# Optimization experiments

Measured on AMD Instinct MI355X. Metric: run time of the kernel, lower is better.

The kernel has to match this reference:

```python
import jax, jax.numpy as jnp
import numpy as np

G = 16       # groups
GRID = 25    # hardcoded self.grid
EPS = 1e-5   # BatchNorm eps


def _gconv(x, w, pad):
    # x: (B, Cin, H, W), w: (Cout, Cin//G, kh, kw); grouped conv, stride 1
    return jax.lax.conv_general_dilated(
        x, w, window_strides=(1, 1), padding=[(pad, pad), (pad, pad)],
        feature_group_count=G)


def _bn_relu(h, g, b, m, v):
    # h: (G, B, C, H, W); per-group-instance BN params: (G, C). Inference BN.
    scale = (g / jnp.sqrt(v + EPS))[:, None, :, None, None]
    return jax.nn.relu((h - m[:, None, :, None, None]) * scale + b[:, None, :, None, None])


def setup_inputs() -> dict:
    key = jax.random.key(0)
    ks = jax.random.split(key, 11)
    B, C, H, W = 2, 256, 24, 24
    AC = GRID * C  # 6400 affinity channels
    return {
        "x":  jax.random.normal(ks[0], (B, C, H, W), jnp.float32),
        "W1": jax.random.normal(ks[1], (G, C, C // G, 3, 3), jnp.float32) * 0.05,
        "g1": jax.random.uniform(ks[2], (G, C), jnp.float32, 0.5, 1.5),
        "b1": jax.random.normal(ks[3], (G, C), jnp.float32) * 0.1,
        "m1": jax.random.normal(ks[4], (G, C), jnp.float32) * 0.1,
        "v1": jax.random.uniform(ks[5], (G, C), jnp.float32, 0.5, 1.5),
        "W2": jax.random.normal(ks[6], (G, AC, C // G, 1, 1), jnp.float32) * 0.05,
        "g2": jax.random.uniform(ks[7], (G, AC), jnp.float32, 0.5, 1.5),
        "b2": jax.random.normal(ks[8], (G, AC), jnp.float32) * 0.1,
        "m2": jax.random.normal(ks[9], (G, AC), jnp.float32) * 0.1,
        "v2": jax.random.uniform(ks[10], (G, AC), jnp.float32, 0.5, 1.5),
    }


def reference(x, W1, g1, b1, m1, v1, W2, g2, b2, m2, v2):
    B, C, H, W = x.shape
    Cg = C // G
    # 16 independent grouped 3x3 convs over the same input, batched via vmap
    h1 = jax.vmap(lambda w: _gconv(x, w, 1))(W1)          # (G, B, C, H, W)
    h1 = _bn_relu(h1, g1, b1, m1, v1)
    # grouped 1x1 conv with padding=1 (faithful to source -> spatial grows to H+2, W+2)
    a = jax.vmap(lambda h, w: _gconv(h, w, 1))(h1, W2)    # (G, B, 25C, H+2, W+2)
    a = _bn_relu(a, g2, b2, m2, v2)
    pooled = a.mean(axis=(-2, -1))                        # adaptive avg pool -> (G, B, 25C)
    xv = pooled.reshape(G, B, G, GRID * Cg)               # (G, B, G, 25*Cg)
    aff = jnp.einsum('ibkm,iblm->ibkl', xv, xv)           # (G, B, G, G) = theta @ phi
    idx = jnp.arange(G)
    aff_i = aff[idx, :, idx, :] / G                       # aff[:, i], /N  -> (G, B, G)
    ex = h1.reshape(G, B, G, Cg * H * W)
    # torch.matmul((B,G), (B,G,M)) broadcasts 2-D lhs -> (B, B, M); kept faithfully
    z = jnp.einsum('ipk,iqkm->ipqm', aff_i, ex)           # (G, B, B, Cg*H*W)
    z = z.reshape(G, B, B, Cg, H, W).transpose(1, 0, 2, 3, 4, 5)
    return z.reshape(B, G * B * Cg, H, W)                 # (B, B*C, H, W)
```

## Files before the change

kernel.cpp:

```cpp
#include <hip/hip_runtime.h>
#include <hip/hip_bf16.h>


typedef __attribute__((ext_vector_type(8))) short short8;
typedef __attribute__((ext_vector_type(4))) float f32x4;

static __device__ __forceinline__ unsigned short f2bf(float x) {
    unsigned u = __float_as_uint(x);
    unsigned r = (u + 0x7fffu + ((u >> 16) & 1u)) >> 16;
    return (unsigned short)r;
}

#define WA_OFF   33696
#define HS_OFF   40096
#define WLB_OFF  63136
#define B2_OFF   75936
#define PACC_OFF 77536
#define S1_OFF   79136
#define BB1_OFF  79200
#define ZP_OFF   79264
#define SMEM_BYTES 79280

__global__ __launch_bounds__(256) void k12_fused(
    const float* __restrict__ xin,
    const float* __restrict__ W1,
    const float* __restrict__ g1, const float* __restrict__ b1,
    const float* __restrict__ m1, const float* __restrict__ v1,
    const float* __restrict__ W2,
    const float* __restrict__ g2, const float* __restrict__ b2,
    const float* __restrict__ m2, const float* __restrict__ v2,
    unsigned short* __restrict__ h1b,
    float* __restrict__ pooled)
{
    __shared__ __align__(16) char smem[SMEM_BYTES];
    short* xs    = (short*)smem;
    short* wAp   = (short*)(smem + WA_OFF);
    short* hsb   = (short*)(smem + HS_OFF);
    short* wlb   = (short*)(smem + WLB_OFF);
    float* bias2 = (float*)(smem + B2_OFF);
    float* pacc  = (float*)(smem + PACC_OFF);
    float* scale1 = (float*)(smem + S1_OFF);
    float* bias1  = (float*)(smem + BB1_OFF);

    int bid = blockIdx.x;
    int i = bid >> 5, b = (bid >> 4) & 1, g = bid & 15;
    int t = threadIdx.x;

    if (t < 16) {
        int c = i*256 + g*16 + t;
        float sc = g1[c] * rsqrtf(v1[c] + 1e-5f);
        scale1[t] = sc;
        bias1[t]  = b1[c] - m1[c] * sc;
    }
    {
        int* xz = (int*)xs;
        for (int idx = t; idx < 1512; idx += 256) {
            int c = idx / 12, j = idx - (idx / 12) * 12;
            int row, col;
            if (c < 26)      { row = 0;  col = c; }
            else if (c < 52) { row = 25; col = c - 26; }
            else if (c < 78) { row = 26; col = c - 52; }
            else { int k = c - 78; row = 1 + (k >> 1); col = (k & 1) ? 25 : 0; }
            xz[(row*26 + col)*12 + j] = 0;
        }
        if (t < 4) ((int*)(smem + ZP_OFF))[t] = 0;
    }
    {
        const float* xb = &xin[(b*256 + g*16)*576];
        for (int idx = t; idx < 9216; idx += 256) {
            int ci = idx / 576; int s = idx - ci*576;
            int y = s / 24; int x = s - y*24;
            xs[((y+1)*26 + (x+1))*24 + ci] = (short)f2bf(xb[idx]);
        }
    }
    {
        const float* wb = &W1[(i*256 + g*16)*144];
        for (int idx = t; idx < 2560; idx += 256) {
            int kk = idx >> 9, rem = idx & 511, co = rem >> 5, k = rem & 31;
            int tap = 2*kk + (k >> 4), ci = k & 15;
            int c = i*256 + g*16 + co;
            float sc = g1[c] * rsqrtf(v1[c] + 1e-5f);
            float val = (tap < 9) ? wb[co*144 + ci*9 + tap] * sc : 0.f;
            wAp[(kk*16 + co)*40 + k] = (short)f2bf(val);
        }
    }
    for (int m = t; m < 400; m += 256) {
        pacc[m] = 0.f;
        int o = i*6400 + g*400 + m;
        float s2 = g2[o] * rsqrtf(v2[o] + 1e-5f);
        bias2[m] = b2[o] - m2[o] * s2;
        const float4* wr = (const float4*)&W2[o*16];
#pragma unroll
        for (int q = 0; q < 4; q++) {
            float4 wv = wr[q];
            wlb[m*16 + q*4 + 0] = (short)f2bf(wv.x * s2);
            wlb[m*16 + q*4 + 1] = (short)f2bf(wv.y * s2);
            wlb[m*16 + q*4 + 2] = (short)f2bf(wv.z * s2);
            wlb[m*16 + q*4 + 3] = (short)f2bf(wv.w * s2);
        }
    }
    __syncthreads();

    int l = t & 63, w = t >> 6;
    int quad = l >> 4, rc = l & 15;

    f32x4 dreg[9];
    {
        int ci0 = (quad & 1) * 8;
        short8 afr[5];
#pragma unroll
        for (int kk = 0; kk < 5; kk++)
            afr[kk] = *(const short8*)&wAp[(kk*16 + rc)*40 + quad*8];
        f32x4 cb1 = *(const f32x4*)&bias1[quad*4];

        const int offE[5] = {0, 48, 648, 1248, 1296};
        const int offO[5] = {24, 624, 672, 1272, 1872};
        int off[5];
#pragma unroll
        for (int kk = 0; kk < 5; kk++) off[kk] = (quad >= 2) ? offO[kk] : offE[kk];

#pragma unroll
        for (int tt = 0; tt < 9; tt++) {
            int s = (w*9 + tt)*16 + rc;
            int y = s / 24; int x = s - y*24;
            int base = (y*26 + x)*24 + ci0;
            f32x4 acc = cb1;
#pragma unroll
            for (int kk = 0; kk < 5; kk++) {
                short8 bf = *(const short8*)&xs[base + off[kk]];
                acc = __builtin_amdgcn_mfma_f32_16x16x32_bf16(afr[kk], bf, acc, 0, 0, 0);
            }
#pragma unroll
            for (int r = 0; r < 4; r++) acc[r] = fmaxf(acc[r], 0.f);
            dreg[tt] = acc;
        }
    }

    {
        unsigned short* hout = &h1b[((i*2 + b)*256 + g*16)*576];
#pragma unroll
        for (int tt = 0; tt < 9; tt++) {
            int s = (w*9 + tt)*16 + rc;
            f32x4 acc = dreg[tt];
            unsigned short e0 = f2bf(acc[0]), e1 = f2bf(acc[1]);
            unsigned short e2 = f2bf(acc[2]), e3 = f2bf(acc[3]);
            uint2 pk = {(unsigned)e0 | ((unsigned)e1 << 16),
                        (unsigned)e2 | ((unsigned)e3 << 16)};
            *(uint2*)&hsb[s*20 + quad*4] = pk;
            hout[(quad*4 + 0)*576 + s] = e0;
            hout[(quad*4 + 1)*576 + s] = e1;
            hout[(quad*4 + 2)*576 + s] = e2;
            hout[(quad*4 + 3)*576 + s] = e3;
        }
    }

    {
        int q8 = (quad & 1) * 8;
        short8 af2[9];
#pragma unroll
        for (int u = 0; u < 9; u++) {
            int boff = (l < 32) ? (HS_OFF + (((w*9 + u)*16 + rc)*20 + q8)*2) : ZP_OFF;
            af2[u] = *(const short8*)(smem + boff);
        }
        for (int mt = 0; mt < 25; mt++) {
            int m0 = mt*16;
            int woff = (l < 32) ? (WLB_OFF + ((m0 + rc)*16 + q8)*2) : ZP_OFF;
            short8 wf = *(const short8*)(smem + woff);
            float be = bias2[m0 + rc];
            f32x4 cb = {be, be, be, be};

            f32x4 accv = {0.f, 0.f, 0.f, 0.f};
#pragma unroll
            for (int u = 0; u < 9; u++) {
                f32x4 d = __builtin_amdgcn_mfma_f32_16x16x32_bf16(af2[u], wf, cb, 0, 0, 0);
#pragma unroll
                for (int r = 0; r < 4; r++)
                    accv[r] += fmaxf(d[r], 0.f);
            }
            float a = (accv[0] + accv[1]) + (accv[2] + accv[3]);
            a += __shfl_xor(a, 16);
            a += __shfl_xor(a, 32);
            if (l < 16)
                atomicAdd(&pacc[m0 + l], a);
        }
    }
    __syncthreads();

    const float inv = 1.f / 676.f;
    for (int m = t; m < 400; m += 256) {
        float be = bias2[m];
        pooled[(i*2+b)*6400 + g*400 + m] =
            (pacc[m] + 100.f * fmaxf(be, 0.f)) * inv;
    }
}

__global__ __launch_bounds__(256) void k3_aff(const float* __restrict__ pooled,
                                              float* __restrict__ aff)
{
    __shared__ float th[400];
    __shared__ float parts[256];
    int bid = blockIdx.x;
    int i = bid >> 1;
    int t = threadIdx.x;
    const float* pb = &pooled[bid*6400];
    for (int idx = t; idx < 400; idx += 256) th[idx] = pb[i*400 + idx];
    __syncthreads();
    int l = t >> 4, p = t & 15;
    float sum = 0.f;
    const float* pl = &pb[l*400];
    for (int m = p*25; m < p*25 + 25; m++) sum = fmaf(th[m], pl[m], sum);
    parts[t] = sum;
    __syncthreads();
    if (t < 16) {
        float s = 0.f;
        for (int pp = 0; pp < 16; pp++) s += parts[t*16 + pp];
        aff[bid*16 + t] = s * (1.f/16.f);
    }
}

__global__ __launch_bounds__(256) void k4_out(const unsigned short* __restrict__ h1b,
                                              const float* __restrict__ aff,
                                              float* __restrict__ out)
{
    __shared__ float a0[16], a1[16];
    int bid = blockIdx.x;
    int i = bid >> 5, q = (bid >> 4) & 1, cg = bid & 15;
    int t = threadIdx.x;
    if (t < 16) a0[t] = aff[(i*2+0)*16 + t];
    else if (t < 32) a1[t-16] = aff[(i*2+1)*16 + (t-16)];
    __syncthreads();
    const unsigned short* hb = &h1b[((i*2+q)*256 + cg)*576];
    int ch = i*32 + q*16 + cg;
    for (int pp = t; pp < 288; pp += 256) {
        int s = pp*2;
        float acc0a = 0.f, acc0b = 0.f, acc1a = 0.f, acc1b = 0.f;
#pragma unroll
        for (int k = 0; k < 16; k++) {
            unsigned hv = *(const unsigned*)&hb[k*9216 + s];
            float va = __uint_as_float(hv << 16);
            float vb = __uint_as_float(hv & 0xffff0000u);
            acc0a = fmaf(a0[k], va, acc0a);
            acc0b = fmaf(a0[k], vb, acc0b);
            acc1a = fmaf(a1[k], va, acc1a);
            acc1b = fmaf(a1[k], vb, acc1b);
        }
        float2 o0 = {acc0a, acc0b};
        float2 o1 = {acc1a, acc1b};
        *(float2*)&out[ch*576 + s]         = o0;
        *(float2*)&out[(512 + ch)*576 + s] = o1;
    }
}

extern "C" void kernel_launch(void* const* d_in, const int* in_sizes, int n_in,
                              void* d_out, int out_size, void* d_ws, size_t ws_size,
                              hipStream_t stream)
{
    const float* x  = (const float*)d_in[0];
    const float* W1 = (const float*)d_in[1];
    const float* g1 = (const float*)d_in[2];
    const float* b1 = (const float*)d_in[3];
    const float* m1 = (const float*)d_in[4];
    const float* v1 = (const float*)d_in[5];
    const float* W2 = (const float*)d_in[6];
    const float* g2 = (const float*)d_in[7];
    const float* b2 = (const float*)d_in[8];
    const float* m2 = (const float*)d_in[9];
    const float* v2 = (const float*)d_in[10];

    unsigned short* h1b = (unsigned short*)d_ws;
    float* pooled = (float*)(h1b + 16*2*256*576);
    float* aff    = pooled + 204800;

    float* out = (float*)d_out;

    hipLaunchKernelGGL(k12_fused, dim3(512), dim3(256), 0, stream,
                       x, W1, g1, b1, m1, v1, W2, g2, b2, m2, v2, h1b, pooled);
    hipLaunchKernelGGL(k3_aff,    dim3(32),  dim3(256), 0, stream,
                       pooled, aff);
    hipLaunchKernelGGL(k4_out,    dim3(512), dim3(256), 0, stream,
                       h1b, aff, out);
}
```

Before: 116.4 us.

## Alias LDS buffers to halve shared memory and prefetch W2 into registers

New measurement: 116.9 us. About the same (+0.5%).

```diff
diff --git a/kernel.cpp b/kernel.cpp
--- a/kernel.cpp
+++ b/kernel.cpp
@@ -12,14 +12,12 @@
 }
 
 #define WA_OFF   33696
-#define HS_OFF   40096
-#define WLB_OFF  63136
-#define B2_OFF   75936
-#define PACC_OFF 77536
-#define S1_OFF   79136
-#define BB1_OFF  79200
-#define ZP_OFF   79264
-#define SMEM_BYTES 79280
+#define WLB_OFF  23040
+#define B2_OFF   35840
+#define PACC_OFF 37440
+#define ZP_OFF   39040
+#define BB1_OFF  40096
+#define SMEM_BYTES 40160
 
 __global__ __launch_bounds__(256) void k12_fused(
     const float* __restrict__ xin,
@@ -35,22 +33,40 @@
     __shared__ __align__(16) char smem[SMEM_BYTES];
     short* xs    = (short*)smem;
     short* wAp   = (short*)(smem + WA_OFF);
-    short* hsb   = (short*)(smem + HS_OFF);
+    short* hsb   = (short*)smem;
     short* wlb   = (short*)(smem + WLB_OFF);
     float* bias2 = (float*)(smem + B2_OFF);
     float* pacc  = (float*)(smem + PACC_OFF);
-    float* scale1 = (float*)(smem + S1_OFF);
-    float* bias1  = (float*)(smem + BB1_OFF);
+    float* bias1 = (float*)(smem + BB1_OFF);
 
     int bid = blockIdx.x;
     int i = bid >> 5, b = (bid >> 4) & 1, g = bid & 15;
     int t = threadIdx.x;
 
+    float4 w2r[2][4];
+    float  bsc[2];
+    {
+#pragma unroll
+        for (int it = 0; it < 2; it++) {
+            int m = t + it*256;
+            bool act = (m < 400);
+            int o = i*6400 + g*400 + (act ? m : 0);
+            float s2 = g2[o] * rsqrtf(v2[o] + 1e-5f);
+            bsc[it] = b2[o] - m2[o] * s2;
+            const float4* wr = (const float4*)&W2[o*16];
+#pragma unroll
+            for (int q = 0; q < 4; q++) {
+                float4 wv = wr[q];
+                wv.x *= s2; wv.y *= s2; wv.z *= s2; wv.w *= s2;
+                w2r[it][q] = wv;
+            }
+        }
+    }
+
     if (t < 16) {
         int c = i*256 + g*16 + t;
         float sc = g1[c] * rsqrtf(v1[c] + 1e-5f);
-        scale1[t] = sc;
-        bias1[t]  = b1[c] - m1[c] * sc;
+        bias1[t] = b1[c] - m1[c] * sc;
     }
     {
         int* xz = (int*)xs;
@@ -63,7 +79,6 @@
             else { int k = c - 78; row = 1 + (k >> 1); col = (k & 1) ? 25 : 0; }
             xz[(row*26 + col)*12 + j] = 0;
         }
-        if (t < 4) ((int*)(smem + ZP_OFF))[t] = 0;
     }
     {
         const float* xb = &xin[(b*256 + g*16)*576];
@@ -84,21 +99,6 @@
             wAp[(kk*16 + co)*40 + k] = (short)f2bf(val);
         }
     }
-    for (int m = t; m < 400; m += 256) {
-        pacc[m] = 0.f;
-        int o = i*6400 + g*400 + m;
-        float s2 = g2[o] * rsqrtf(v2[o] + 1e-5f);
-        bias2[m] = b2[o] - m2[o] * s2;
-        const float4* wr = (const float4*)&W2[o*16];
-#pragma unroll
-        for (int q = 0; q < 4; q++) {
-            float4 wv = wr[q];
-            wlb[m*16 + q*4 + 0] = (short)f2bf(wv.x * s2);
-            wlb[m*16 + q*4 + 1] = (short)f2bf(wv.y * s2);
-            wlb[m*16 + q*4 + 2] = (short)f2bf(wv.z * s2);
-            wlb[m*16 + q*4 + 3] = (short)f2bf(wv.w * s2);
-        }
-    }
     __syncthreads();
 
     int l = t & 63, w = t >> 6;
@@ -135,6 +135,7 @@
             dreg[tt] = acc;
         }
     }
+    __syncthreads();
 
     {
         unsigned short* hout = &h1b[((i*2 + b)*256 + g*16)*576];
@@ -153,13 +154,31 @@
             hout[(quad*4 + 3)*576 + s] = e3;
         }
     }
+#pragma unroll
+    for (int it = 0; it < 2; it++) {
+        int m = t + it*256;
+        if (m < 400) {
+            pacc[m]  = 0.f;
+            bias2[m] = bsc[it];
+#pragma unroll
+            for (int q = 0; q < 4; q++) {
+                float4 wv = w2r[it][q];
+                wlb[m*16 + q*4 + 0] = (short)f2bf(wv.x);
+                wlb[m*16 + q*4 + 1] = (short)f2bf(wv.y);
+                wlb[m*16 + q*4 + 2] = (short)f2bf(wv.z);
+                wlb[m*16 + q*4 + 3] = (short)f2bf(wv.w);
+            }
+        }
+    }
+    if (t < 4) ((int*)(smem + ZP_OFF))[t] = 0;
+    __syncthreads();
 
     {
         int q8 = (quad & 1) * 8;
         short8 af2[9];
 #pragma unroll
         for (int u = 0; u < 9; u++) {
-            int boff = (l < 32) ? (HS_OFF + (((w*9 + u)*16 + rc)*20 + q8)*2) : ZP_OFF;
+            int boff = (l < 32) ? ((((w*9 + u)*16 + rc)*20 + q8)*2) : ZP_OFF;
             af2[u] = *(const short8*)(smem + boff);
         }
         for (int mt = 0; mt < 25; mt++) {
@@ -229,26 +248,29 @@
     if (t < 16) a0[t] = aff[(i*2+0)*16 + t];
     else if (t < 32) a1[t-16] = aff[(i*2+1)*16 + (t-16)];
     __syncthreads();
+    if (t >= 144) return;
     const unsigned short* hb = &h1b[((i*2+q)*256 + cg)*576];
     int ch = i*32 + q*16 + cg;
-    for (int pp = t; pp < 288; pp += 256) {
-        int s = pp*2;
-        float acc0a = 0.f, acc0b = 0.f, acc1a = 0.f, acc1b = 0.f;
-#pragma unroll
-        for (int k = 0; k < 16; k++) {
-            unsigned hv = *(const unsigned*)&hb[k*9216 + s];
-            float va = __uint_as_float(hv << 16);
-            float vb = __uint_as_float(hv & 0xffff0000u);
-            acc0a = fmaf(a0[k], va, acc0a);
-            acc0b = fmaf(a0[k], vb, acc0b);
-            acc1a = fmaf(a1[k], va, acc1a);
-            acc1b = fmaf(a1[k], vb, acc1b);
-        }
-        float2 o0 = {acc0a, acc0b};
-        float2 o1 = {acc1a, acc1b};
-        *(float2*)&out[ch*576 + s]         = o0;
-        *(float2*)&out[(512 + ch)*576 + s] = o1;
-    }
+    int s = t*4;
+    float c00=0.f,c01=0.f,c02=0.f,c03=0.f;
+    float c10=0.f,c11=0.f,c12=0.f,c13=0.f;
+#pragma unroll
+    for (int k = 0; k < 16; k++) {
+        uint2 hv = *(const uint2*)&hb[k*9216 + s];
+        float p0 = __uint_as_float(hv.x << 16);
+        float p1 = __uint_as_float(hv.x & 0xffff0000u);
+        float p2 = __uint_as_float(hv.y << 16);
+        float p3 = __uint_as_float(hv.y & 0xffff0000u);
+        float va = a0[k], vb = a1[k];
+        c00 = fmaf(va, p0, c00); c01 = fmaf(va, p1, c01);
+        c02 = fmaf(va, p2, c02); c03 = fmaf(va, p3, c03);
+        c10 = fmaf(vb, p0, c10); c11 = fmaf(vb, p1, c11);
+        c12 = fmaf(vb, p2, c12); c13 = fmaf(vb, p3, c13);
+    }
+    float4 o0 = {c00, c01, c02, c03};
+    float4 o1 = {c10, c11, c12, c13};
+    *(float4*)&out[ch*576 + s]         = o0;
+    *(float4*)&out[(512 + ch)*576 + s] = o1;
 }
 
 extern "C" void kernel_launch(void* const* d_in, const int* in_sizes, int n_in,
```
